# Kernel tuning notes

Measured on AMD Instinct MI355X. Metric: run time of the kernel, lower is better.

The kernel has to match this reference:

```python
import jax, jax.numpy as jnp
import numpy as np

GROUPS = 8   # channels // group_size with group_size=8 for C=64
EPS = 1e-5


def group_norm_qc(x0, x1, gamma, beta):
    """LatticeGroupNorm: stats computed jointly over both cosets per (batch, group)."""
    B, C, H, W = x0.shape
    g = GROUPS
    xg = jnp.concatenate([x0.reshape(B, g, -1), x1.reshape(B, g, -1)], axis=-1)
    mean = xg.mean(axis=-1).reshape(B, g, 1, 1, 1)
    var = xg.var(axis=-1).reshape(B, g, 1, 1, 1)
    inv = jax.lax.rsqrt(var + EPS)
    ga = gamma[None, :, None, None]
    be = beta[None, :, None, None]

    def norm(x):
        xr = x.reshape(B, g, C // g, H, W)
        return ((xr - mean) * inv).reshape(B, C, H, W) * ga + be

    return norm(x0), norm(x1)


def qc_conv(x0, x1, w_center, w_corner, bias):
    """Quincunx LatticePad+LatticeConvolution with stencil
    [(0,0),(2,0),(0,2),(2,2),(1,1)], center (1,1).
    w_center: [O,I] tap (1,1) (same-coset 1x1).
    w_corner: [O,I,2,2] taps (0,0),(2,0),(0,2),(2,2) (cross-coset 2x2).
    Pad keeps output cosets the same size as inputs ('same' lattice conv)."""
    dn = ('NCHW', 'OIHW', 'NCHW')

    def c1(x):
        return jnp.einsum('oi,bihw->bohw', w_center, x)

    def c2(x, pad):
        return jax.lax.conv_general_dilated(x, w_corner, (1, 1), pad,
                                            dimension_numbers=dn)

    b = bias[None, :, None, None]
    # coset0 output gathers coset1 at (i-1+a, j-1+b) -> pad top/left
    out0 = c1(x0) + c2(x1, ((1, 0), (1, 0))) + b
    # coset1 output gathers coset0 at (i+a, j+b) -> pad bottom/right
    out1 = c1(x1) + c2(x0, ((0, 1), (0, 1))) + b
    return out0, out1


def setup_inputs() -> dict:
    key = jax.random.key(0)
    ks = jax.random.split(key, 10)
    B, C, H, W = 2, 64, 256, 256
    s = 0.05
    return {
        'x0': jax.random.normal(ks[0], (B, C, H, W), jnp.float32),
        'x1': jax.random.normal(ks[1], (B, C, H, W), jnp.float32),
        'g1': jnp.ones((C,), jnp.float32),
        'b1': jnp.zeros((C,), jnp.float32),
        'w1_center': jax.random.normal(ks[2], (C, C), jnp.float32) * s,
        'w1_corner': jax.random.normal(ks[3], (C, C, 2, 2), jnp.float32) * s,
        'bias1': jax.random.normal(ks[4], (C,), jnp.float32) * s,
        'g2': jnp.ones((C,), jnp.float32),
        'b2': jnp.zeros((C,), jnp.float32),
        'w2_center': jax.random.normal(ks[5], (C, C), jnp.float32) * s,
        'w2_corner': jax.random.normal(ks[6], (C, C, 2, 2), jnp.float32) * s,
        'bias2': jax.random.normal(ks[7], (C,), jnp.float32) * s,
        'w_skip': jax.random.normal(ks[8], (C, C), jnp.float32) * s,
        'bias_skip': jax.random.normal(ks[9], (C,), jnp.float32) * s,
        'g_skip': jnp.ones((C,), jnp.float32),
        'beta_skip': jnp.zeros((C,), jnp.float32),
    }


def reference(x0, x1, g1, b1, w1_center, w1_corner, bias1,
              g2, b2, w2_center, w2_corner, bias2,
              w_skip, bias_skip, g_skip, beta_skip):
    # conv path: GN -> ReLU -> pad+conv -> GN -> ReLU -> pad+conv
    h0, h1 = group_norm_qc(x0, x1, g1, b1)
    h0, h1 = jax.nn.relu(h0), jax.nn.relu(h1)
    h0, h1 = qc_conv(h0, h1, w1_center, w1_corner, bias1)
    h0, h1 = group_norm_qc(h0, h1, g2, b2)
    h0, h1 = jax.nn.relu(h0), jax.nn.relu(h1)
    h0, h1 = qc_conv(h0, h1, w2_center, w2_corner, bias2)
    # skip path: 1x1 lattice conv (stencil [(0,0)]) -> GN
    bsk = bias_skip[None, :, None, None]
    s0 = jnp.einsum('oi,bihw->bohw', w_skip, x0) + bsk
    s1 = jnp.einsum('oi,bihw->bohw', w_skip, x1) + bsk
    s0, s1 = group_norm_qc(s0, s1, g_skip, beta_skip)
    # residual add; stack the two cosets as leading axis for a single output
    return jnp.stack([h0 + s0, h1 + s1])
```

## Files before the change

### kernel.cpp

```cpp
#include <hip/hip_runtime.h>

typedef __attribute__((ext_vector_type(8))) __bf16 bf16x8;
typedef __attribute__((ext_vector_type(4))) __bf16 bf16x4;
typedef __attribute__((ext_vector_type(4))) float f32x4;

#define MFMA16(a,b,c) __builtin_amdgcn_mfma_f32_16x16x32_bf16(a,b,c,0,0,0)

static constexpr int HW = 65536;
static constexpr int WD = 256;
static constexpr int NB = 2;
static constexpr double INV_N = 1.0 / 1048576.0;
static constexpr float EPSV = 1e-5f;

static constexpr size_t OFF_P1  = 0;
static constexpr size_t OFF_P2  = 131072;
static constexpr size_t OFF_A1  = 200704;
static constexpr size_t OFF_A2  = OFF_A1 + 40960;
static constexpr size_t OFF_XT  = OFF_A2 + 40960;
static constexpr size_t SZ_T    = (size_t)2 * NB * HW * 64 * 2;
static constexpr size_t OFF_S   = OFF_XT + SZ_T;
static constexpr size_t OFF_H   = OFF_S + SZ_T;

#define TL8(base, px, c) (*(const bf16x8*)&(base)[(px) * 64 + (((c)) ^ ((((px)) & 7) << 3))])

__global__ __launch_bounds__(256, 4) void K1(
    const float* __restrict__ x0, const float* __restrict__ x1,
    const float* __restrict__ wskip, const float* __restrict__ bskip,
    const float* __restrict__ wc1, const float* __restrict__ wk1,
    const float* __restrict__ wc2, const float* __restrict__ wk2,
    __bf16* __restrict__ xt, __bf16* __restrict__ sout,
    __bf16* __restrict__ A1, __bf16* __restrict__ A2, float* __restrict__ p1) {
  const int bx = blockIdx.x;
  const int t = threadIdx.x;

  if (bx >= 1024) {
    const int stage = bx - 1024;
    const float* wc = stage ? wc2 : wc1;
    const float* wk = stage ? wk2 : wk1;
    __bf16* A = stage ? A2 : A1;
    for (int idx = t; idx < 64 * 320; idx += 256) {
      int o = idx / 320, k = idx - o * 320;
      float v;
      if (k < 64) v = wc[o * 64 + k];
      else {
        int tp = (k - 64) >> 6;
        int c = k & 63;
        v = wk[(o * 64 + c) * 4 + tp];
      }
      A[idx] = (__bf16)v;
    }
    return;
  }

  const int row = bx & 255;
  const int b   = (bx >> 8) & 1;
  const int co  = bx >> 9;
  const float* x = co ? x1 : x0;
  __shared__ __attribute__((aligned(16))) __bf16 tile[256 * 64];
  __shared__ float redp[256];
  __shared__ float reds[32];
  const int wv = t >> 6, lane = t & 63;

  const float* xbase = x + (size_t)b * 64 * HW + (size_t)row * WD + t;
  __bf16* xtbase = xt + (((size_t)(co * NB + b) * HW) + (size_t)row * WD + t) * 64;

  float gsum[8], gsq[8];
#pragma unroll
  for (int g = 0; g < 8; ++g) { gsum[g] = 0.f; gsq[g] = 0.f; }
#pragma unroll
  for (int hf = 0; hf < 2; ++hf) {
    float f[32];
#pragma unroll
    for (int k = 0; k < 32; ++k) f[k] = xbase[(size_t)(hf * 32 + k) * HW];
    __builtin_amdgcn_sched_barrier(0);
#pragma unroll
    for (int c4 = 0; c4 < 4; ++c4) {
      const int cg = hf * 4 + c4;
      bf16x8 v;
#pragma unroll
      for (int j = 0; j < 8; ++j) {
        float xv = f[c4 * 8 + j];
        v[j] = (__bf16)xv;
        gsum[cg] += xv;
        gsq[cg] = fmaf(xv, xv, gsq[cg]);
      }
      *(bf16x8*)&tile[t * 64 + ((cg ^ (t & 7)) * 8)] = v;
      *(bf16x8*)&xtbase[cg * 8] = v;
    }
  }
#pragma unroll
  for (int g = 0; g < 8; ++g) {
#pragma unroll
    for (int m = 1; m < 16; m <<= 1) {
      gsum[g] += __shfl_xor(gsum[g], m, 64);
      gsq[g]  += __shfl_xor(gsq[g], m, 64);
    }
  }
  {
    const int q0 = lane >> 4;
    if ((lane & 15) == 0) {
#pragma unroll
      for (int g = 0; g < 8; ++g) {
        redp[(wv * 4 + q0) * 16 + g] = gsum[g];
        redp[(wv * 4 + q0) * 16 + 8 + g] = gsq[g];
      }
    }
  }
  __syncthreads();

  const int ln = lane & 15, q = lane >> 4;
  const int ch0 = wv * 16 + q * 4;
  bf16x8 a0, a1;
#pragma unroll
  for (int j = 0; j < 8; ++j) {
    a0[j] = (__bf16)wskip[(wv * 16 + ln) * 64 + q * 8 + j];
    a1[j] = (__bf16)wskip[(wv * 16 + ln) * 64 + 32 + q * 8 + j];
  }
  float bia[4];
#pragma unroll
  for (int r = 0; r < 4; ++r) bia[r] = bskip[ch0 + r];

  float ssum = 0.f, ssq = 0.f;
  for (int n = 0; n < 16; ++n) {
    f32x4 acc = {0.f, 0.f, 0.f, 0.f};
    const int px = n * 16 + ln;
    bf16x8 b0 = TL8(tile, px, q * 8);
    bf16x8 b1 = TL8(tile, px, q * 8 + 32);
    acc = MFMA16(a0, b0, acc);
    acc = MFMA16(a1, b1, acc);
    bf16x4 sv;
    float v[4];
#pragma unroll
    for (int r = 0; r < 4; ++r) {
      v[r] = acc[r] + bia[r];
      ssum += v[r];
      ssq = fmaf(v[r], v[r], ssq);
      sv[r] = (__bf16)v[r];
    }
    size_t sb = ((size_t)(co * NB + b) * 4096 + row * 16 + n) * 1024 + (wv * 4 + q) * 64 + ln * 4;
    *(bf16x4*)&sout[sb] = sv;
  }
#pragma unroll
  for (int m = 1; m < 16; m <<= 1) {
    ssum += __shfl_xor(ssum, m, 64);
    ssq  += __shfl_xor(ssq, m, 64);
  }
  if ((lane & 15) == 0) {
    reds[wv * 4 + q] = ssum;
    reds[16 + wv * 4 + q] = ssq;
  }

  __syncthreads();
  if (t < 32) {
    float val;
    if (t < 16) {
      val = 0.f;
#pragma unroll
      for (int k = 0; k < 16; ++k) val += redp[k * 16 + t];
    } else {
      int kind = (t >> 3) & 1, g = t & 7;
      int wvv = g >> 1, qp = g & 1;
      val = reds[kind * 16 + wvv * 4 + qp * 2] + reds[kind * 16 + wvv * 4 + qp * 2 + 1];
    }
    const int bf1 = (co * 2 + b) * 256 + row;
    p1[(size_t)bf1 * 32 + t] = val;
  }
}

__global__ __launch_bounds__(256, 4) void K2(
    const __bf16* __restrict__ xt, const __bf16* __restrict__ A1,
    const float* __restrict__ p1, const float* __restrict__ g1, const float* __restrict__ be1,
    const float* __restrict__ bias1,
    __bf16* __restrict__ h, float* __restrict__ p2) {
  const int blk = ((blockIdx.x & 7) << 6) | (blockIdx.x >> 3);
  const int tx = blk & 15, ty = blk >> 4;
  const int b = blockIdx.y;
  const int y0p = ty * 8, x0p = tx * 16;
  __shared__ __attribute__((aligned(16))) __bf16 tl[2][153 * 64];
  __shared__ float sc[64], sh[64];
  __shared__ float lst[16];
  __shared__ double redn[16];
  const int t = threadIdx.x;

  bf16x8 raw[10];
#pragma unroll
  for (int i = 0; i < 10; ++i) {
    int u = t + i * 256;
    int cs = (u >= 1224) ? 1 : 0;
    int rr = u - cs * 1224;
    int px = rr >> 3, cg = rr & 7;
    int ly = px / 17, lx = px - ly * 17;
    int gy = y0p + ly - cs, gx = x0p + lx - cs;
    if (u < 2448 && (unsigned)gy < 256u && (unsigned)gx < 256u)
      raw[i] = *(const bf16x8*)&xt[(((size_t)(cs * NB + b) * WD + gy) * WD + gx) * 64 + cg * 8];
  }
  __builtin_amdgcn_sched_barrier(0);

  if (t < 16) lst[t] = 0.f;
  {
    const int col = t >> 4, sub = t & 15;
    double v = 0.0;
    for (int j = sub; j < 512; j += 16) {
      int cc = j >> 8, rr2 = j & 255;
      v += (double)p1[((size_t)(cc * 2 + b) * 256 + rr2) * 32 + col];
    }
    v += __shfl_xor(v, 1, 64);
    v += __shfl_xor(v, 2, 64);
    v += __shfl_xor(v, 4, 64);
    v += __shfl_xor(v, 8, 64);
    if (sub == 0) redn[col] = v;
  }
  __syncthreads();
  if (t < 64) {
    int g = t >> 3;
    double mean = redn[g] * INV_N;
    double var  = redn[8 + g] * INV_N - mean * mean;
    float inv = rsqrtf((float)var + EPSV);
    float s_ = inv * g1[t];
    sc[t] = s_;
    sh[t] = be1[t] - (float)mean * s_;
  }
  __syncthreads();

#pragma unroll
  for (int i = 0; i < 10; ++i) {
    int u = t + i * 256;
    int cs = (u >= 1224) ? 1 : 0;
    int rr = u - cs * 1224;
    int px = rr >> 3, cg = rr & 7;
    int ly = px / 17, lx = px - ly * 17;
    int gy = y0p + ly - cs, gx = x0p + lx - cs;
    if (u < 2448) {
      bool inb = (unsigned)gy < 256u && (unsigned)gx < 256u;
      bf16x8 v;
#pragma unroll
      for (int j = 0; j < 8; ++j) {
        float fv = inb ? fmaf((float)raw[i][j], sc[cg * 8 + j], sh[cg * 8 + j]) : 0.f;
        v[j] = (__bf16)fmaxf(fv, 0.f);
      }
      *(bf16x8*)&tl[cs][px * 64 + ((cg ^ (px & 7)) * 8)] = v;
    }
  }

  const int wv = t >> 6, lane = t & 63, ln = lane & 15, q = lane >> 4;
  const int co = wv & 1, mh = wv >> 1;
  const int q8 = q * 8;
  bf16x8 af[2][10];
#pragma unroll
  for (int m = 0; m < 2; ++m)
#pragma unroll
    for (int kk = 0; kk < 10; ++kk)
      af[m][kk] = *(const bf16x8*)&A1[(mh * 32 + m * 16 + ln) * 320 + kk * 32 + q8];
  __syncthreads();

  f32x4 acc[8][2];
#pragma unroll
  for (int n = 0; n < 8; ++n)
#pragma unroll
    for (int m = 0; m < 2; ++m) acc[n][m] = (f32x4){0.f, 0.f, 0.f, 0.f};

  const __bf16* tc = tl[co];
  const __bf16* to = tl[1 - co];
#pragma unroll
  for (int n = 0; n < 8; ++n) {
    const int cpix = co ? ((n + 1) * 17 + ln + 1) : (n * 17 + ln);
    const int tb = n * 17 + ln;
    bf16x8 bb;
    bb = TL8(tc, cpix, q8);          acc[n][0]=MFMA16(af[0][0],bb,acc[n][0]); acc[n][1]=MFMA16(af[1][0],bb,acc[n][1]);
    bb = TL8(tc, cpix, q8 + 32);     acc[n][0]=MFMA16(af[0][1],bb,acc[n][0]); acc[n][1]=MFMA16(af[1][1],bb,acc[n][1]);
    bb = TL8(to, tb, q8);            acc[n][0]=MFMA16(af[0][2],bb,acc[n][0]); acc[n][1]=MFMA16(af[1][2],bb,acc[n][1]);
    bb = TL8(to, tb, q8 + 32);       acc[n][0]=MFMA16(af[0][3],bb,acc[n][0]); acc[n][1]=MFMA16(af[1][3],bb,acc[n][1]);
    bb = TL8(to, tb + 1, q8);        acc[n][0]=MFMA16(af[0][4],bb,acc[n][0]); acc[n][1]=MFMA16(af[1][4],bb,acc[n][1]);
    bb = TL8(to, tb + 1, q8 + 32);   acc[n][0]=MFMA16(af[0][5],bb,acc[n][0]); acc[n][1]=MFMA16(af[1][5],bb,acc[n][1]);
    bb = TL8(to, tb + 17, q8);       acc[n][0]=MFMA16(af[0][6],bb,acc[n][0]); acc[n][1]=MFMA16(af[1][6],bb,acc[n][1]);
    bb = TL8(to, tb + 17, q8 + 32);  acc[n][0]=MFMA16(af[0][7],bb,acc[n][0]); acc[n][1]=MFMA16(af[1][7],bb,acc[n][1]);
    bb = TL8(to, tb + 18, q8);       acc[n][0]=MFMA16(af[0][8],bb,acc[n][0]); acc[n][1]=MFMA16(af[1][8],bb,acc[n][1]);
    bb = TL8(to, tb + 18, q8 + 32);  acc[n][0]=MFMA16(af[0][9],bb,acc[n][0]); acc[n][1]=MFMA16(af[1][9],bb,acc[n][1]);
  }

  __syncthreads();

  float s2s[2] = {0.f, 0.f}, s2q[2] = {0.f, 0.f};
  float bia[2][4];
#pragma unroll
  for (int m = 0; m < 2; ++m)
#pragma unroll
    for (int r = 0; r < 4; ++r) bia[m][r] = bias1[mh * 32 + m * 16 + q * 4 + r];

#pragma unroll
  for (int n = 0; n < 8; ++n)
#pragma unroll
    for (int m = 0; m < 2; ++m) {
      bf16x4 hv;
#pragma unroll
      for (int r = 0; r < 4; ++r) {
        float v = acc[n][m][r] + bia[m][r];
        s2s[m] += v;
        s2q[m] = fmaf(v, v, s2q[m]);
        hv[r] = (__bf16)v;
      }
      *(bf16x4*)&tl[co][(n * 16 + ln) * 64 + ((mh * 32 + m * 16 + q * 4) ^ ((ln & 7) << 3))] = hv;
    }

#pragma unroll
  for (int m = 0; m < 2; ++m) {
    float a_ = s2s[m], c_ = s2q[m];
#pragma unroll
    for (int mk = 1; mk < 32; mk <<= 1) {
      a_ += __shfl_xor(a_, mk, 64);
      c_ += __shfl_xor(c_, mk, 64);
    }
    if ((lane & 31) == 0) {
      int g = mh * 4 + m * 2 + (q >> 1);
      atomicAdd(&lst[g], a_);
      atomicAdd(&lst[8 + g], c_);
    }
  }
  __syncthreads();

#pragma unroll
  for (int i = 0; i < 8; ++i) {
    int co2 = i >> 2;
    int idx = (i & 3) * 256 + t;
    int px = idx >> 3, chunk = idx & 7;
    int gy = y0p + (px >> 4), gx = x0p + (px & 15);
    bf16x8 vv = *(const bf16x8*)&tl[co2][px * 64 + ((chunk ^ (px & 7)) * 8)];
    *(bf16x8*)&h[(((size_t)(co2 * NB + b) * WD + gy) * WD + gx) * 64 + chunk * 8] = vv;
  }

  if (t < 16) p2[((size_t)b * 512 + blockIdx.x) * 16 + t] = lst[t];
}

__global__ __launch_bounds__(256, 4) void K3(
    const __bf16* __restrict__ hin, const __bf16* __restrict__ A2,
    const float* __restrict__ p2, const float* __restrict__ p1,
    const float* __restrict__ g2, const float* __restrict__ be2, const float* __restrict__ bias2,
    const float* __restrict__ gsk, const float* __restrict__ besk,
    const __bf16* __restrict__ sin_, float* __restrict__ out) {
  const int blk = ((blockIdx.x & 7) << 6) | (blockIdx.x >> 3);
  const int tx = blk & 15, ty = blk >> 4;
  const int b = blockIdx.y;
  const int y0p = ty * 8, x0p = tx * 16;
  __shared__ __attribute__((aligned(16))) __bf16 tl[2][153 * 64];
  __shared__ float sc2[64], sh2[64], scS[64], shS[64];
  __shared__ double redn[32];
  const int t = threadIdx.x;

  bf16x8 raw[10];
#pragma unroll
  for (int i = 0; i < 10; ++i) {
    int u = t + i * 256;
    int cs = (u >= 1224) ? 1 : 0;
    int rr = u - cs * 1224;
    int px = rr >> 3, cg = rr & 7;
    int ly = px / 17, lx = px - ly * 17;
    int gy = y0p + ly - cs, gx = x0p + lx - cs;
    if (u < 2448 && (unsigned)gy < 256u && (unsigned)gx < 256u)
      raw[i] = *(const bf16x8*)&hin[(((size_t)(cs * NB + b) * WD + gy) * WD + gx) * 64 + cg * 8];
  }
  __builtin_amdgcn_sched_barrier(0);

  {
    const int col = t >> 3, sub = t & 7;
    double v = 0.0;
    if (col < 16) {
      for (int j = sub; j < 512; j += 8)
        v += (double)p2[((size_t)b * 512 + j) * 16 + col];
    } else {
      for (int j = sub; j < 512; j += 8) {
        int cc = j >> 8, rr2 = j & 255;
        v += (double)p1[((size_t)(cc * 2 + b) * 256 + rr2) * 32 + col];
      }
    }
    v += __shfl_xor(v, 1, 64);
    v += __shfl_xor(v, 2, 64);
    v += __shfl_xor(v, 4, 64);
    if (sub == 0) redn[col] = v;
  }
  __syncthreads();
  if (t < 128) {
    int half = t >> 6, ch = t & 63, g = ch >> 3;
    if (half == 0) {
      double mean = redn[g] * INV_N;
      double var  = redn[8 + g] * INV_N - mean * mean;
      float inv = rsqrtf((float)var + EPSV);
      float s_ = inv * g2[ch];
      sc2[ch] = s_;
      sh2[ch] = be2[ch] - (float)mean * s_;
    } else {
      double mean = redn[16 + g] * INV_N;
      double var  = redn[24 + g] * INV_N - mean * mean;
      float inv = rsqrtf((float)var + EPSV);
      float s_ = inv * gsk[ch];
      scS[ch] = s_;
      shS[ch] = besk[ch] - (float)mean * s_;
    }
  }
  __syncthreads();

#pragma unroll
  for (int i = 0; i < 10; ++i) {
    int u = t + i * 256;
    int cs = (u >= 1224) ? 1 : 0;
    int rr = u - cs * 1224;
    int px = rr >> 3, cg = rr & 7;
    int ly = px / 17, lx = px - ly * 17;
    int gy = y0p + ly - cs, gx = x0p + lx - cs;
    if (u < 2448) {
      bool inb = (unsigned)gy < 256u && (unsigned)gx < 256u;
      bf16x8 v;
#pragma unroll
      for (int j = 0; j < 8; ++j) {
        float fv = inb ? fmaf((float)raw[i][j], sc2[cg * 8 + j], sh2[cg * 8 + j]) : 0.f;
        v[j] = (__bf16)fmaxf(fv, 0.f);
      }
      *(bf16x8*)&tl[cs][px * 64 + ((cg ^ (px & 7)) * 8)] = v;
    }
  }

  const int wv = t >> 6, lane = t & 63, ln = lane & 15, q = lane >> 4;
  const int co = wv & 1, mh = wv >> 1;
  const int q8 = q * 8;
  bf16x8 af[2][10];
#pragma unroll
  for (int m = 0; m < 2; ++m)
#pragma unroll
    for (int kk = 0; kk < 10; ++kk)
      af[m][kk] = *(const bf16x8*)&A2[(mh * 32 + m * 16 + ln) * 320 + kk * 32 + q8];
  __syncthreads();

  f32x4 acc[8][2];
#pragma unroll
  for (int n = 0; n < 8; ++n)
#pragma unroll
    for (int m = 0; m < 2; ++m) acc[n][m] = (f32x4){0.f, 0.f, 0.f, 0.f};

  const __bf16* tc = tl[co];
  const __bf16* to = tl[1 - co];
#pragma unroll
  for (int n = 0; n < 8; ++n) {
    const int cpix = co ? ((n + 1) * 17 + ln + 1) : (n * 17 + ln);
    const int tb = n * 17 + ln;
    bf16x8 bb;
    bb = TL8(tc, cpix, q8);          acc[n][0]=MFMA16(af[0][0],bb,acc[n][0]); acc[n][1]=MFMA16(af[1][0],bb,acc[n][1]);
    bb = TL8(tc, cpix, q8 + 32);     acc[n][0]=MFMA16(af[0][1],bb,acc[n][0]); acc[n][1]=MFMA16(af[1][1],bb,acc[n][1]);
    bb = TL8(to, tb, q8);            acc[n][0]=MFMA16(af[0][2],bb,acc[n][0]); acc[n][1]=MFMA16(af[1][2],bb,acc[n][1]);
    bb = TL8(to, tb, q8 + 32);       acc[n][0]=MFMA16(af[0][3],bb,acc[n][0]); acc[n][1]=MFMA16(af[1][3],bb,acc[n][1]);
    bb = TL8(to, tb + 1, q8);        acc[n][0]=MFMA16(af[0][4],bb,acc[n][0]); acc[n][1]=MFMA16(af[1][4],bb,acc[n][1]);
    bb = TL8(to, tb + 1, q8 + 32);   acc[n][0]=MFMA16(af[0][5],bb,acc[n][0]); acc[n][1]=MFMA16(af[1][5],bb,acc[n][1]);
    bb = TL8(to, tb + 17, q8);       acc[n][0]=MFMA16(af[0][6],bb,acc[n][0]); acc[n][1]=MFMA16(af[1][6],bb,acc[n][1]);
    bb = TL8(to, tb + 17, q8 + 32);  acc[n][0]=MFMA16(af[0][7],bb,acc[n][0]); acc[n][1]=MFMA16(af[1][7],bb,acc[n][1]);
    bb = TL8(to, tb + 18, q8);       acc[n][0]=MFMA16(af[0][8],bb,acc[n][0]); acc[n][1]=MFMA16(af[1][8],bb,acc[n][1]);
    bb = TL8(to, tb + 18, q8 + 32);  acc[n][0]=MFMA16(af[0][9],bb,acc[n][0]); acc[n][1]=MFMA16(af[1][9],bb,acc[n][1]);
  }

  float bia[2][4], sA[2][4], sB[2][4];
#pragma unroll
  for (int m = 0; m < 2; ++m)
#pragma unroll
    for (int r = 0; r < 4; ++r) {
      int ch = mh * 32 + m * 16 + q * 4 + r;
      bia[m][r] = bias2[ch];
      sA[m][r] = scS[ch];
      sB[m][r] = shS[ch];
    }

#pragma unroll
  for (int ng = 0; ng < 2; ++ng) {
    bf16x4 sv[4][2];
#pragma unroll
    for (int nn = 0; nn < 4; ++nn) {
      int n = ng * 4 + nn;
      int gy = y0p + n;
#pragma unroll
      for (int m = 0; m < 2; ++m)
        sv[nn][m] = *(const bf16x4*)&sin_[((size_t)(co * NB + b) * 4096 + gy * 16 + tx) * 1024 + (mh * 8 + m * 4 + q) * 64 + ln * 4];
    }
    __builtin_amdgcn_sched_barrier(0);
#pragma unroll
    for (int nn = 0; nn < 4; ++nn) {
      int n = ng * 4 + nn;
      int gy = y0p + n;
#pragma unroll
      for (int m = 0; m < 2; ++m) {
        int ch0 = mh * 32 + m * 16 + q * 4;
        size_t ob = ((size_t)(co * NB + b) * 64 + ch0) * HW + (size_t)gy * WD + x0p + ln;
#pragma unroll
        for (int r = 0; r < 4; ++r) {
          float v = acc[n][m][r] + bia[m][r] + fmaf((float)sv[nn][m][r], sA[m][r], sB[m][r]);
          out[ob + (size_t)r * HW] = v;
        }
      }
    }
  }
}

extern "C" void kernel_launch(void* const* d_in, const int* in_sizes, int n_in,
                              void* d_out, int out_size, void* d_ws, size_t ws_size,
                              hipStream_t stream) {
  (void)in_sizes; (void)n_in; (void)out_size; (void)ws_size;
  const float* x0    = (const float*)d_in[0];
  const float* x1    = (const float*)d_in[1];
  const float* g1    = (const float*)d_in[2];
  const float* b1    = (const float*)d_in[3];
  const float* w1c   = (const float*)d_in[4];
  const float* w1k   = (const float*)d_in[5];
  const float* bias1 = (const float*)d_in[6];
  const float* g2    = (const float*)d_in[7];
  const float* b2    = (const float*)d_in[8];
  const float* w2c   = (const float*)d_in[9];
  const float* w2k   = (const float*)d_in[10];
  const float* bias2 = (const float*)d_in[11];
  const float* wsk   = (const float*)d_in[12];
  const float* bsk   = (const float*)d_in[13];
  const float* gsk   = (const float*)d_in[14];
  const float* besk  = (const float*)d_in[15];

  char* ws = (char*)d_ws;
  float*  p1 = (float*)(ws + OFF_P1);
  float*  p2 = (float*)(ws + OFF_P2);
  __bf16* A1 = (__bf16*)(ws + OFF_A1);
  __bf16* A2 = (__bf16*)(ws + OFF_A2);
  __bf16* xt = (__bf16*)(ws + OFF_XT);
  __bf16* s  = (__bf16*)(ws + OFF_S);
  __bf16* h  = (__bf16*)(ws + OFF_H);

  K1<<<dim3(1026), 256, 0, stream>>>(x0, x1, wsk, bsk, w1c, w1k, w2c, w2k, xt, s, A1, A2, p1);
  K2<<<dim3(512, 2), 256, 0, stream>>>(xt, A1, p1, g1, b1, bias1, h, p2);
  K3<<<dim3(512, 2), 256, 0, stream>>>(h, A2, p2, p1, g2, b2, bias2, gsk, besk, s, (float*)d_out);
}
```

Baseline: 309.1 us.

## Fuse three kernels into one cooperative persistent kernel with grid syncs

Adds a cooperative kernel KF that runs the stats/skip-conv stage, the first GN+conv stage and the second GN+conv+residual stage in a single launch. The stages are separated by grid.sync() and share one reused shared-memory buffer. Weight repacking is spread across all blocks instead of two extra blocks. The goal is to remove launch gaps and kernel-boundary drains between the three stages, at the cost of grid-barrier overhead. It also requires all 1024 blocks to be co-resident (4 per CU), and falls back to the old three-kernel path otherwise.

```diff
diff --git a/kernel.cpp b/kernel.cpp
--- a/kernel.cpp
+++ b/kernel.cpp
@@ -1,4 +1,7 @@
 #include <hip/hip_runtime.h>
+#include <hip/hip_cooperative_groups.h>
+
+namespace cg = cooperative_groups;
 
 typedef __attribute__((ext_vector_type(8))) __bf16 bf16x8;
 typedef __attribute__((ext_vector_type(4))) __bf16 bf16x4;
@@ -22,6 +25,459 @@
 static constexpr size_t OFF_H   = OFF_S + SZ_T;
 
 #define TL8(base, px, c) (*(const bf16x8*)&(base)[(px) * 64 + (((c)) ^ ((((px)) & 7) << 3))])
+
+__global__ __launch_bounds__(256, 4) void KF(
+    const float* __restrict__ x0, const float* __restrict__ x1,
+    const float* __restrict__ wskip, const float* __restrict__ bskip,
+    const float* __restrict__ wc1, const float* __restrict__ wk1,
+    const float* __restrict__ wc2, const float* __restrict__ wk2,
+    const float* __restrict__ g1, const float* __restrict__ be1, const float* __restrict__ bias1,
+    const float* __restrict__ g2, const float* __restrict__ be2, const float* __restrict__ bias2,
+    const float* __restrict__ gsk, const float* __restrict__ besk,
+    __bf16* __restrict__ xt, __bf16* __restrict__ sout, __bf16* __restrict__ h,
+    __bf16* __restrict__ A1, __bf16* __restrict__ A2,
+    float* __restrict__ p1, float* __restrict__ p2, float* __restrict__ out) {
+  cg::grid_group grid = cg::this_grid();
+  __shared__ __attribute__((aligned(16))) char smem[40448];
+  const int bx = blockIdx.x;
+  const int t = threadIdx.x;
+  const int wv = t >> 6, lane = t & 63;
+  const int ln = lane & 15, q = lane >> 4;
+  const int q8 = q * 8;
+
+  {
+    __bf16* tile = (__bf16*)smem;
+    float* redp  = (float*)(smem + 32768);
+    float* reds  = (float*)(smem + 33792);
+
+    if (t < 40) {
+      int e = bx * 40 + t;
+      int stage = e / 20480, idx = e - stage * 20480;
+      const float* wc = stage ? wc2 : wc1;
+      const float* wk = stage ? wk2 : wk1;
+      int o = idx / 320, k = idx - o * 320;
+      float v = (k < 64) ? wc[o * 64 + k] : wk[(o * 64 + (k & 63)) * 4 + ((k - 64) >> 6)];
+      (stage ? A2 : A1)[idx] = (__bf16)v;
+    }
+
+    const int row = bx & 255, b = (bx >> 8) & 1, co = bx >> 9;
+    const float* x = co ? x1 : x0;
+    const float* xbase = x + (size_t)b * 64 * HW + (size_t)row * WD + t;
+    __bf16* xtbase = xt + (((size_t)(co * NB + b) * HW) + (size_t)row * WD + t) * 64;
+
+    float gsum[8], gsq[8];
+#pragma unroll
+    for (int g = 0; g < 8; ++g) { gsum[g] = 0.f; gsq[g] = 0.f; }
+#pragma unroll
+    for (int hf = 0; hf < 2; ++hf) {
+      float f[32];
+#pragma unroll
+      for (int k = 0; k < 32; ++k) f[k] = xbase[(size_t)(hf * 32 + k) * HW];
+      __builtin_amdgcn_sched_barrier(0);
+#pragma unroll
+      for (int c4 = 0; c4 < 4; ++c4) {
+        const int cgi = hf * 4 + c4;
+        bf16x8 v;
+#pragma unroll
+        for (int j = 0; j < 8; ++j) {
+          float xv = f[c4 * 8 + j];
+          v[j] = (__bf16)xv;
+          gsum[cgi] += xv;
+          gsq[cgi] = fmaf(xv, xv, gsq[cgi]);
+        }
+        *(bf16x8*)&tile[t * 64 + ((cgi ^ (t & 7)) * 8)] = v;
+        *(bf16x8*)&xtbase[cgi * 8] = v;
+      }
+    }
+#pragma unroll
+    for (int g = 0; g < 8; ++g) {
+#pragma unroll
+      for (int m = 1; m < 16; m <<= 1) {
+        gsum[g] += __shfl_xor(gsum[g], m, 64);
+        gsq[g]  += __shfl_xor(gsq[g], m, 64);
+      }
+    }
+    if ((lane & 15) == 0) {
+#pragma unroll
+      for (int g = 0; g < 8; ++g) {
+        redp[(wv * 4 + q) * 16 + g] = gsum[g];
+        redp[(wv * 4 + q) * 16 + 8 + g] = gsq[g];
+      }
+    }
+    __syncthreads();
+
+    bf16x8 a0, a1;
+#pragma unroll
+    for (int j = 0; j < 8; ++j) {
+      a0[j] = (__bf16)wskip[(wv * 16 + ln) * 64 + q * 8 + j];
+      a1[j] = (__bf16)wskip[(wv * 16 + ln) * 64 + 32 + q * 8 + j];
+    }
+    float bia[4];
+#pragma unroll
+    for (int r = 0; r < 4; ++r) bia[r] = bskip[wv * 16 + q * 4 + r];
+
+    float ssum = 0.f, ssq = 0.f;
+    for (int n = 0; n < 16; ++n) {
+      f32x4 acc = {0.f, 0.f, 0.f, 0.f};
+      const int px = n * 16 + ln;
+      bf16x8 b0 = TL8(tile, px, q * 8);
+      bf16x8 b1 = TL8(tile, px, q * 8 + 32);
+      acc = MFMA16(a0, b0, acc);
+      acc = MFMA16(a1, b1, acc);
+      bf16x4 sv;
+#pragma unroll
+      for (int r = 0; r < 4; ++r) {
+        float v = acc[r] + bia[r];
+        ssum += v;
+        ssq = fmaf(v, v, ssq);
+        sv[r] = (__bf16)v;
+      }
+      size_t sb = ((size_t)(co * NB + b) * 4096 + row * 16 + n) * 1024 + (wv * 4 + q) * 64 + ln * 4;
+      *(bf16x4*)&sout[sb] = sv;
+    }
+#pragma unroll
+    for (int m = 1; m < 16; m <<= 1) {
+      ssum += __shfl_xor(ssum, m, 64);
+      ssq  += __shfl_xor(ssq, m, 64);
+    }
+    if ((lane & 15) == 0) {
+      reds[wv * 4 + q] = ssum;
+      reds[16 + wv * 4 + q] = ssq;
+    }
+    __syncthreads();
+    if (t < 32) {
+      float val;
+      if (t < 16) {
+        val = 0.f;
+#pragma unroll
+        for (int k = 0; k < 16; ++k) val += redp[k * 16 + t];
+      } else {
+        int kind = (t >> 3) & 1, g = t & 7;
+        int wvv = g >> 1, qp = g & 1;
+        val = reds[kind * 16 + wvv * 4 + qp * 2] + reds[kind * 16 + wvv * 4 + qp * 2 + 1];
+      }
+      p1[(size_t)((co * 2 + b) * 256 + row) * 32 + t] = val;
+    }
+  }
+
+  grid.sync();
+
+  const int gidx = ((bx & 7) << 7) | (bx >> 3);
+  const int b23 = gidx >> 9, r23 = gidx & 511;
+  const int tx = r23 & 15, ty = r23 >> 4;
+  const int y0p = ty * 8, x0p = tx * 16;
+  __bf16* tl0 = (__bf16*)smem;
+  __bf16* tl1 = tl0 + 153 * 64;
+
+  {
+    float* sc   = (float*)(smem + 39168);
+    float* sh   = (float*)(smem + 39424);
+    float* lst  = (float*)(smem + 39680);
+    double* redn = (double*)(smem + 39744);
+
+    bf16x8 raw[10];
+#pragma unroll
+    for (int i = 0; i < 10; ++i) {
+      int u = t + i * 256;
+      int cs = (u >= 1224) ? 1 : 0;
+      int rr = u - cs * 1224;
+      int px = rr >> 3, cgi = rr & 7;
+      int ly = px / 17, lx = px - ly * 17;
+      int gy = y0p + ly - cs, gx = x0p + lx - cs;
+      if (u < 2448 && (unsigned)gy < 256u && (unsigned)gx < 256u)
+        raw[i] = *(const bf16x8*)&xt[(((size_t)(cs * NB + b23) * WD + gy) * WD + gx) * 64 + cgi * 8];
+    }
+    __builtin_amdgcn_sched_barrier(0);
+
+    if (t < 16) lst[t] = 0.f;
+    {
+      const int col = t >> 4, sub = t & 15;
+      double v = 0.0;
+      for (int j = sub; j < 512; j += 16) {
+        int cc = j >> 8, rr2 = j & 255;
+        v += (double)p1[((size_t)(cc * 2 + b23) * 256 + rr2) * 32 + col];
+      }
+      v += __shfl_xor(v, 1, 64);
+      v += __shfl_xor(v, 2, 64);
+      v += __shfl_xor(v, 4, 64);
+      v += __shfl_xor(v, 8, 64);
+      if (sub == 0) redn[col] = v;
+    }
+    __syncthreads();
+    if (t < 64) {
+      int g = t >> 3;
+      double mean = redn[g] * INV_N;
+      double var  = redn[8 + g] * INV_N - mean * mean;
+      float inv = rsqrtf((float)var + EPSV);
+      float s_ = inv * g1[t];
+      sc[t] = s_;
+      sh[t] = be1[t] - (float)mean * s_;
+    }
+    __syncthreads();
+
+#pragma unroll
+    for (int i = 0; i < 10; ++i) {
+      int u = t + i * 256;
+      int cs = (u >= 1224) ? 1 : 0;
+      int rr = u - cs * 1224;
+      int px = rr >> 3, cgi = rr & 7;
+      int ly = px / 17, lx = px - ly * 17;
+      int gy = y0p + ly - cs, gx = x0p + lx - cs;
+      if (u < 2448) {
+        bool inb = (unsigned)gy < 256u && (unsigned)gx < 256u;
+        bf16x8 v;
+#pragma unroll
+        for (int j = 0; j < 8; ++j) {
+          float fv = inb ? fmaf((float)raw[i][j], sc[cgi * 8 + j], sh[cgi * 8 + j]) : 0.f;
+          v[j] = (__bf16)fmaxf(fv, 0.f);
+        }
+        *(bf16x8*)&(cs ? tl1 : tl0)[px * 64 + ((cgi ^ (px & 7)) * 8)] = v;
+      }
+    }
+
+    const int co = wv & 1, mh = wv >> 1;
+    bf16x8 af[2][10];
+#pragma unroll
+    for (int m = 0; m < 2; ++m)
+#pragma unroll
+      for (int kk = 0; kk < 10; ++kk)
+        af[m][kk] = *(const bf16x8*)&A1[(mh * 32 + m * 16 + ln) * 320 + kk * 32 + q8];
+    __syncthreads();
+
+    f32x4 acc[8][2];
+#pragma unroll
+    for (int n = 0; n < 8; ++n)
+#pragma unroll
+      for (int m = 0; m < 2; ++m) acc[n][m] = (f32x4){0.f, 0.f, 0.f, 0.f};
+
+    const __bf16* tc = co ? tl1 : tl0;
+    const __bf16* to = co ? tl0 : tl1;
+#pragma unroll
+    for (int n = 0; n < 8; ++n) {
+      const int cpix = co ? ((n + 1) * 17 + ln + 1) : (n * 17 + ln);
+      const int tb = n * 17 + ln;
+      bf16x8 bb;
+      bb = TL8(tc, cpix, q8);          acc[n][0]=MFMA16(af[0][0],bb,acc[n][0]); acc[n][1]=MFMA16(af[1][0],bb,acc[n][1]);
+      bb = TL8(tc, cpix, q8 + 32);     acc[n][0]=MFMA16(af[0][1],bb,acc[n][0]); acc[n][1]=MFMA16(af[1][1],bb,acc[n][1]);
+      bb = TL8(to, tb, q8);            acc[n][0]=MFMA16(af[0][2],bb,acc[n][0]); acc[n][1]=MFMA16(af[1][2],bb,acc[n][1]);
+      bb = TL8(to, tb, q8 + 32);       acc[n][0]=MFMA16(af[0][3],bb,acc[n][0]); acc[n][1]=MFMA16(af[1][3],bb,acc[n][1]);
+      bb = TL8(to, tb + 1, q8);        acc[n][0]=MFMA16(af[0][4],bb,acc[n][0]); acc[n][1]=MFMA16(af[1][4],bb,acc[n][1]);
+      bb = TL8(to, tb + 1, q8 + 32);   acc[n][0]=MFMA16(af[0][5],bb,acc[n][0]); acc[n][1]=MFMA16(af[1][5],bb,acc[n][1]);
+      bb = TL8(to, tb + 17, q8);       acc[n][0]=MFMA16(af[0][6],bb,acc[n][0]); acc[n][1]=MFMA16(af[1][6],bb,acc[n][1]);
+      bb = TL8(to, tb + 17, q8 + 32);  acc[n][0]=MFMA16(af[0][7],bb,acc[n][0]); acc[n][1]=MFMA16(af[1][7],bb,acc[n][1]);
+      bb = TL8(to, tb + 18, q8);       acc[n][0]=MFMA16(af[0][8],bb,acc[n][0]); acc[n][1]=MFMA16(af[1][8],bb,acc[n][1]);
+      bb = TL8(to, tb + 18, q8 + 32);  acc[n][0]=MFMA16(af[0][9],bb,acc[n][0]); acc[n][1]=MFMA16(af[1][9],bb,acc[n][1]);
+    }
+
+    __syncthreads();
+
+    float s2s[2] = {0.f, 0.f}, s2q[2] = {0.f, 0.f};
+    float bia[2][4];
+#pragma unroll
+    for (int m = 0; m < 2; ++m)
+#pragma unroll
+      for (int r = 0; r < 4; ++r) bia[m][r] = bias1[mh * 32 + m * 16 + q * 4 + r];
+
+#pragma unroll
+    for (int n = 0; n < 8; ++n)
+#pragma unroll
+      for (int m = 0; m < 2; ++m) {
+        bf16x4 hv;
+#pragma unroll
+        for (int r = 0; r < 4; ++r) {
+          float v = acc[n][m][r] + bia[m][r];
+          s2s[m] += v;
+          s2q[m] = fmaf(v, v, s2q[m]);
+          hv[r] = (__bf16)v;
+        }
+        *(bf16x4*)&(co ? tl1 : tl0)[(n * 16 + ln) * 64 + ((mh * 32 + m * 16 + q * 4) ^ ((ln & 7) << 3))] = hv;
+      }
+
+#pragma unroll
+    for (int m = 0; m < 2; ++m) {
+      float a_ = s2s[m], c_ = s2q[m];
+#pragma unroll
+      for (int mk = 1; mk < 32; mk <<= 1) {
+        a_ += __shfl_xor(a_, mk, 64);
+        c_ += __shfl_xor(c_, mk, 64);
+      }
+      if ((lane & 31) == 0) {
+        int g = mh * 4 + m * 2 + (q >> 1);
+        atomicAdd(&lst[g], a_);
+        atomicAdd(&lst[8 + g], c_);
+      }
+    }
+    __syncthreads();
+
+#pragma unroll
+    for (int i = 0; i < 8; ++i) {
+      int co2 = i >> 2;
+      int idx = (i & 3) * 256 + t;
+      int px = idx >> 3, chunk = idx & 7;
+      int gy = y0p + (px >> 4), gx = x0p + (px & 15);
+      bf16x8 vv = *(const bf16x8*)&(co2 ? tl1 : tl0)[px * 64 + ((chunk ^ (px & 7)) * 8)];
+      *(bf16x8*)&h[(((size_t)(co2 * NB + b23) * WD + gy) * WD + gx) * 64 + chunk * 8] = vv;
+    }
+
+    if (t < 16) p2[((size_t)b23 * 512 + r23) * 16 + t] = lst[t];
+  }
+
+  grid.sync();
+
+  {
+    float* sc2  = (float*)(smem + 39168);
+    float* sh2  = (float*)(smem + 39424);
+    float* scS  = (float*)(smem + 39680);
+    float* shS  = (float*)(smem + 39936);
+    double* redn = (double*)(smem + 40192);
+
+    bf16x8 raw[10];
+#pragma unroll
+    for (int i = 0; i < 10; ++i) {
+      int u = t + i * 256;
+      int cs = (u >= 1224) ? 1 : 0;
+      int rr = u - cs * 1224;
+      int px = rr >> 3, cgi = rr & 7;
+      int ly = px / 17, lx = px - ly * 17;
+      int gy = y0p + ly - cs, gx = x0p + lx - cs;
+      if (u < 2448 && (unsigned)gy < 256u && (unsigned)gx < 256u)
+        raw[i] = *(const bf16x8*)&h[(((size_t)(cs * NB + b23) * WD + gy) * WD + gx) * 64 + cgi * 8];
+    }
+    __builtin_amdgcn_sched_barrier(0);
+
+    {
+      const int col = t >> 3, sub = t & 7;
+      double v = 0.0;
+      if (col < 16) {
+        for (int j = sub; j < 512; j += 8)
+          v += (double)p2[((size_t)b23 * 512 + j) * 16 + col];
+      } else {
+        for (int j = sub; j < 512; j += 8) {
+          int cc = j >> 8, rr2 = j & 255;
+          v += (double)p1[((size_t)(cc * 2 + b23) * 256 + rr2) * 32 + col];
+        }
+      }
+      v += __shfl_xor(v, 1, 64);
+      v += __shfl_xor(v, 2, 64);
+      v += __shfl_xor(v, 4, 64);
+      if (sub == 0) redn[col] = v;
+    }
+    __syncthreads();
+    if (t < 128) {
+      int half = t >> 6, ch = t & 63, g = ch >> 3;
+      if (half == 0) {
+        double mean = redn[g] * INV_N;
+        double var  = redn[8 + g] * INV_N - mean * mean;
+        float inv = rsqrtf((float)var + EPSV);
+        float s_ = inv * g2[ch];
+        sc2[ch] = s_;
+        sh2[ch] = be2[ch] - (float)mean * s_;
+      } else {
+        double mean = redn[16 + g] * INV_N;
+        double var  = redn[24 + g] * INV_N - mean * mean;
+        float inv = rsqrtf((float)var + EPSV);
+        float s_ = inv * gsk[ch];
+        scS[ch] = s_;
+        shS[ch] = besk[ch] - (float)mean * s_;
+      }
+    }
+    __syncthreads();
+
+#pragma unroll
+    for (int i = 0; i < 10; ++i) {
+      int u = t + i * 256;
+      int cs = (u >= 1224) ? 1 : 0;
+      int rr = u - cs * 1224;
+      int px = rr >> 3, cgi = rr & 7;
+      int ly = px / 17, lx = px - ly * 17;
+      int gy = y0p + ly - cs, gx = x0p + lx - cs;
+      if (u < 2448) {
+        bool inb = (unsigned)gy < 256u && (unsigned)gx < 256u;
+        bf16x8 v;
+#pragma unroll
+        for (int j = 0; j < 8; ++j) {
+          float fv = inb ? fmaf((float)raw[i][j], sc2[cgi * 8 + j], sh2[cgi * 8 + j]) : 0.f;
+          v[j] = (__bf16)fmaxf(fv, 0.f);
+        }
+        *(bf16x8*)&(cs ? tl1 : tl0)[px * 64 + ((cgi ^ (px & 7)) * 8)] = v;
+      }
+    }
+
+    const int co = wv & 1, mh = wv >> 1;
+    bf16x8 af[2][10];
+#pragma unroll
+    for (int m = 0; m < 2; ++m)
+#pragma unroll
+      for (int kk = 0; kk < 10; ++kk)
+        af[m][kk] = *(const bf16x8*)&A2[(mh * 32 + m * 16 + ln) * 320 + kk * 32 + q8];
+    __syncthreads();
+
+    f32x4 acc[8][2];
+#pragma unroll
+    for (int n = 0; n < 8; ++n)
+#pragma unroll
+      for (int m = 0; m < 2; ++m) acc[n][m] = (f32x4){0.f, 0.f, 0.f, 0.f};
+
+    const __bf16* tc = co ? tl1 : tl0;
+    const __bf16* to = co ? tl0 : tl1;
+#pragma unroll
+    for (int n = 0; n < 8; ++n) {
+      const int cpix = co ? ((n + 1) * 17 + ln + 1) : (n * 17 + ln);
+      const int tb = n * 17 + ln;
+      bf16x8 bb;
+      bb = TL8(tc, cpix, q8);          acc[n][0]=MFMA16(af[0][0],bb,acc[n][0]); acc[n][1]=MFMA16(af[1][0],bb,acc[n][1]);
+      bb = TL8(tc, cpix, q8 + 32);     acc[n][0]=MFMA16(af[0][1],bb,acc[n][0]); acc[n][1]=MFMA16(af[1][1],bb,acc[n][1]);
+      bb = TL8(to, tb, q8);            acc[n][0]=MFMA16(af[0][2],bb,acc[n][0]); acc[n][1]=MFMA16(af[1][2],bb,acc[n][1]);
+      bb = TL8(to, tb, q8 + 32);       acc[n][0]=MFMA16(af[0][3],bb,acc[n][0]); acc[n][1]=MFMA16(af[1][3],bb,acc[n][1]);
+      bb = TL8(to, tb + 1, q8);        acc[n][0]=MFMA16(af[0][4],bb,acc[n][0]); acc[n][1]=MFMA16(af[1][4],bb,acc[n][1]);
+      bb = TL8(to, tb + 1, q8 + 32);   acc[n][0]=MFMA16(af[0][5],bb,acc[n][0]); acc[n][1]=MFMA16(af[1][5],bb,acc[n][1]);
+      bb = TL8(to, tb + 17, q8);       acc[n][0]=MFMA16(af[0][6],bb,acc[n][0]); acc[n][1]=MFMA16(af[1][6],bb,acc[n][1]);
+      bb = TL8(to, tb + 17, q8 + 32);  acc[n][0]=MFMA16(af[0][7],bb,acc[n][0]); acc[n][1]=MFMA16(af[1][7],bb,acc[n][1]);
+      bb = TL8(to, tb + 18, q8);       acc[n][0]=MFMA16(af[0][8],bb,acc[n][0]); acc[n][1]=MFMA16(af[1][8],bb,acc[n][1]);
+      bb = TL8(to, tb + 18, q8 + 32);  acc[n][0]=MFMA16(af[0][9],bb,acc[n][0]); acc[n][1]=MFMA16(af[1][9],bb,acc[n][1]);
+    }
+
+    float bia[2][4], sA[2][4], sB[2][4];
+#pragma unroll
+    for (int m = 0; m < 2; ++m)
+#pragma unroll
+      for (int r = 0; r < 4; ++r) {
+        int ch = mh * 32 + m * 16 + q * 4 + r;
+        bia[m][r] = bias2[ch];
+        sA[m][r] = scS[ch];
+        sB[m][r] = shS[ch];
+      }
+
+#pragma unroll
+    for (int ng = 0; ng < 2; ++ng) {
+      bf16x4 sv[4][2];
+#pragma unroll
+      for (int nn = 0; nn < 4; ++nn) {
+        int n = ng * 4 + nn;
+        int gy = y0p + n;
+#pragma unroll
+        for (int m = 0; m < 2; ++m)
+          sv[nn][m] = *(const bf16x4*)&sout[((size_t)(co * NB + b23) * 4096 + gy * 16 + tx) * 1024 + (mh * 8 + m * 4 + q) * 64 + ln * 4];
+      }
+      __builtin_amdgcn_sched_barrier(0);
+#pragma unroll
+      for (int nn = 0; nn < 4; ++nn) {
+        int n = ng * 4 + nn;
+        int gy = y0p + n;
+#pragma unroll
+        for (int m = 0; m < 2; ++m) {
+          int ch0 = mh * 32 + m * 16 + q * 4;
+          size_t ob = ((size_t)(co * NB + b23) * 64 + ch0) * HW + (size_t)gy * WD + x0p + ln;
+#pragma unroll
+          for (int r = 0; r < 4; ++r) {
+            float v = acc[n][m][r] + bia[m][r] + fmaf((float)sv[nn][m][r], sA[m][r], sB[m][r]);
+            out[ob + (size_t)r * HW] = v;
+          }
+        }
+      }
+    }
+  }
+}
 
 __global__ __launch_bounds__(256, 4) void K1(
     const float* __restrict__ x0, const float* __restrict__ x1,
@@ -32,7 +488,6 @@
     __bf16* __restrict__ A1, __bf16* __restrict__ A2, float* __restrict__ p1) {
   const int bx = blockIdx.x;
   const int t = threadIdx.x;
-
   if (bx >= 1024) {
     const int stage = bx - 1024;
     const float* wc = stage ? wc2 : wc1;
@@ -42,28 +497,19 @@
       int o = idx / 320, k = idx - o * 320;
       float v;
       if (k < 64) v = wc[o * 64 + k];
-      else {
-        int tp = (k - 64) >> 6;
-        int c = k & 63;
-        v = wk[(o * 64 + c) * 4 + tp];
-      }
+      else v = wk[(o * 64 + (k & 63)) * 4 + ((k - 64) >> 6)];
       A[idx] = (__bf16)v;
     }
     return;
   }
-
-  const int row = bx & 255;
-  const int b   = (bx >> 8) & 1;
-  const int co  = bx >> 9;
+  const int row = bx & 255, b = (bx >> 8) & 1, co = bx >> 9;
   const float* x = co ? x1 : x0;
   __shared__ __attribute__((aligned(16))) __bf16 tile[256 * 64];
   __shared__ float redp[256];
   __shared__ float reds[32];
   const int wv = t >> 6, lane = t & 63;
-
   const float* xbase = x + (size_t)b * 64 * HW + (size_t)row * WD + t;
   __bf16* xtbase = xt + (((size_t)(co * NB + b) * HW) + (size_t)row * WD + t) * 64;
-
   float gsum[8], gsq[8];
 #pragma unroll
   for (int g = 0; g < 8; ++g) { gsum[g] = 0.f; gsq[g] = 0.f; }
@@ -107,9 +553,7 @@
     }
   }
   __syncthreads();
-
   const int ln = lane & 15, q = lane >> 4;
-  const int ch0 = wv * 16 + q * 4;
   bf16x8 a0, a1;
 #pragma unroll
   for (int j = 0; j < 8; ++j) {
@@ -118,8 +562,7 @@
   }
   float bia[4];
 #pragma unroll
-  for (int r = 0; r < 4; ++r) bia[r] = bskip[ch0 + r];
-
+  for (int r = 0; r < 4; ++r) bia[r] = bskip[wv * 16 + q * 4 + r];
   float ssum = 0.f, ssq = 0.f;
   for (int n = 0; n < 16; ++n) {
     f32x4 acc = {0.f, 0.f, 0.f, 0.f};
@@ -129,13 +572,12 @@
     acc = MFMA16(a0, b0, acc);
     acc = MFMA16(a1, b1, acc);
     bf16x4 sv;
-    float v[4];
 #pragma unroll
     for (int r = 0; r < 4; ++r) {
-      v[r] = acc[r] + bia[r];
-      ssum += v[r];
-      ssq = fmaf(v[r], v[r], ssq);
-      sv[r] = (__bf16)v[r];
+      float v = acc[r] + bia[r];
+      ssum += v;
+      ssq = fmaf(v, v, ssq);
+      sv[r] = (__bf16)v;
     }
     size_t sb = ((size_t)(co * NB + b) * 4096 + row * 16 + n) * 1024 + (wv * 4 + q) * 64 + ln * 4;
     *(bf16x4*)&sout[sb] = sv;
@@ -149,7 +591,6 @@
     reds[wv * 4 + q] = ssum;
     reds[16 + wv * 4 + q] = ssq;
   }
-
   __syncthreads();
   if (t < 32) {
     float val;
@@ -162,8 +603,7 @@
       int wvv = g >> 1, qp = g & 1;
       val = reds[kind * 16 + wvv * 4 + qp * 2] + reds[kind * 16 + wvv * 4 + qp * 2 + 1];
     }
-    const int bf1 = (co * 2 + b) * 256 + row;
-    p1[(size_t)bf1 * 32 + t] = val;
+    p1[(size_t)((co * 2 + b) * 256 + row) * 32 + t] = val;
   }
 }
 
@@ -181,7 +621,6 @@
   __shared__ float lst[16];
   __shared__ double redn[16];
   const int t = threadIdx.x;
-
   bf16x8 raw[10];
 #pragma unroll
   for (int i = 0; i < 10; ++i) {
@@ -195,7 +634,6 @@
       raw[i] = *(const bf16x8*)&xt[(((size_t)(cs * NB + b) * WD + gy) * WD + gx) * 64 + cg * 8];
   }
   __builtin_amdgcn_sched_barrier(0);
-
   if (t < 16) lst[t] = 0.f;
   {
     const int col = t >> 4, sub = t & 15;
@@ -221,7 +659,6 @@
     sh[t] = be1[t] - (float)mean * s_;
   }
   __syncthreads();
-
 #pragma unroll
   for (int i = 0; i < 10; ++i) {
     int u = t + i * 256;
@@ -241,7 +678,6 @@
       *(bf16x8*)&tl[cs][px * 64 + ((cg ^ (px & 7)) * 8)] = v;
     }
   }
-
   const int wv = t >> 6, lane = t & 63, ln = lane & 15, q = lane >> 4;
   const int co = wv & 1, mh = wv >> 1;
   const int q8 = q * 8;
@@ -252,13 +688,11 @@
     for (int kk = 0; kk < 10; ++kk)
       af[m][kk] = *(const bf16x8*)&A1[(mh * 32 + m * 16 + ln) * 320 + kk * 32 + q8];
   __syncthreads();
-
   f32x4 acc[8][2];
 #pragma unroll
   for (int n = 0; n < 8; ++n)
 #pragma unroll
     for (int m = 0; m < 2; ++m) acc[n][m] = (f32x4){0.f, 0.f, 0.f, 0.f};
-
   const __bf16* tc = tl[co];
   const __bf16* to = tl[1 - co];
 #pragma unroll
@@ -277,16 +711,13 @@
     bb = TL8(to, tb + 18, q8);       acc[n][0]=MFMA16(af[0][8],bb,acc[n][0]); acc[n][1]=MFMA16(af[1][8],bb,acc[n][1]);
     bb = TL8(to, tb + 18, q8 + 32);  acc[n][0]=MFMA16(af[0][9],bb,acc[n][0]); acc[n][1]=MFMA16(af[1][9],bb,acc[n][1]);
   }
-
   __syncthreads();
-
   float s2s[2] = {0.f, 0.f}, s2q[2] = {0.f, 0.f};
   float bia[2][4];
 #pragma unroll
   for (int m = 0; m < 2; ++m)
 #pragma unroll
     for (int r = 0; r < 4; ++r) bia[m][r] = bias1[mh * 32 + m * 16 + q * 4 + r];
-
 #pragma unroll
   for (int n = 0; n < 8; ++n)
 #pragma unroll
@@ -301,7 +732,6 @@
       }
       *(bf16x4*)&tl[co][(n * 16 + ln) * 64 + ((mh * 32 + m * 16 + q * 4) ^ ((ln & 7) << 3))] = hv;
     }
-
 #pragma unroll
   for (int m = 0; m < 2; ++m) {
     float a_ = s2s[m], c_ = s2q[m];
@@ -317,7 +747,6 @@
     }
   }
   __syncthreads();
-
 #pragma unroll
   for (int i = 0; i < 8; ++i) {
     int co2 = i >> 2;
@@ -327,7 +756,6 @@
     bf16x8 vv = *(const bf16x8*)&tl[co2][px * 64 + ((chunk ^ (px & 7)) * 8)];
     *(bf16x8*)&h[(((size_t)(co2 * NB + b) * WD + gy) * WD + gx) * 64 + chunk * 8] = vv;
   }
-
   if (t < 16) p2[((size_t)b * 512 + blockIdx.x) * 16 + t] = lst[t];
 }
 
@@ -345,7 +773,6 @@
   __shared__ float sc2[64], sh2[64], scS[64], shS[64];
   __shared__ double redn[32];
   const int t = threadIdx.x;
-
   bf16x8 raw[10];
 #pragma unroll
   for (int i = 0; i < 10; ++i) {
@@ -359,7 +786,6 @@
       raw[i] = *(const bf16x8*)&hin[(((size_t)(cs * NB + b) * WD + gy) * WD + gx) * 64 + cg * 8];
   }
   __builtin_amdgcn_sched_barrier(0);
-
   {
     const int col = t >> 3, sub = t & 7;
     double v = 0.0;
@@ -397,7 +823,6 @@
     }
   }
   __syncthreads();
-
 #pragma unroll
   for (int i = 0; i < 10; ++i) {
     int u = t + i * 256;
@@ -417,7 +842,6 @@
       *(bf16x8*)&tl[cs][px * 64 + ((cg ^ (px & 7)) * 8)] = v;
     }
   }
-
   const int wv = t >> 6, lane = t & 63, ln = lane & 15, q = lane >> 4;
   const int co = wv & 1, mh = wv >> 1;
   const int q8 = q * 8;
@@ -428,13 +852,11 @@
     for (int kk = 0; kk < 10; ++kk)
       af[m][kk] = *(const bf16x8*)&A2[(mh * 32 + m * 16 + ln) * 320 + kk * 32 + q8];
   __syncthreads();
-
   f32x4 acc[8][2];
 #pragma unroll
   for (int n = 0; n < 8; ++n)
 #pragma unroll
     for (int m = 0; m < 2; ++m) acc[n][m] = (f32x4){0.f, 0.f, 0.f, 0.f};
-
   const __bf16* tc = tl[co];
   const __bf16* to = tl[1 - co];
 #pragma unroll
@@ -453,7 +875,6 @@
     bb = TL8(to, tb + 18, q8);       acc[n][0]=MFMA16(af[0][8],bb,acc[n][0]); acc[n][1]=MFMA16(af[1][8],bb,acc[n][1]);
     bb = TL8(to, tb + 18, q8 + 32);  acc[n][0]=MFMA16(af[0][9],bb,acc[n][0]); acc[n][1]=MFMA16(af[1][9],bb,acc[n][1]);
   }
-
   float bia[2][4], sA[2][4], sB[2][4];
 #pragma unroll
   for (int m = 0; m < 2; ++m)
@@ -464,7 +885,6 @@
       sA[m][r] = scS[ch];
       sB[m][r] = shS[ch];
     }
-
 #pragma unroll
   for (int ng = 0; ng < 2; ++ng) {
     bf16x4 sv[4][2];
@@ -524,8 +944,32 @@
   __bf16* xt = (__bf16*)(ws + OFF_XT);
   __bf16* s  = (__bf16*)(ws + OFF_S);
   __bf16* h  = (__bf16*)(ws + OFF_H);
+  float* outp = (float*)d_out;
+
+  static int coopOK = -1;
+  if (coopOK < 0) {
+    int nb = 0;
+    hipError_t e = hipOccupancyMaxActiveBlocksPerMultiprocessor(&nb, KF, 256, 0);
+    coopOK = (e == hipSuccess && nb >= 4) ? 1 : 0;
+  }
+
+  if (coopOK) {
+    void* kargs[] = {
+      (void*)&x0, (void*)&x1, (void*)&wsk, (void*)&bsk,
+      (void*)&w1c, (void*)&w1k, (void*)&w2c, (void*)&w2k,
+      (void*)&g1, (void*)&b1, (void*)&bias1,
+      (void*)&g2, (void*)&b2, (void*)&bias2,
+      (void*)&gsk, (void*)&besk,
+      (void*)&xt, (void*)&s, (void*)&h, (void*)&A1, (void*)&A2,
+      (void*)&p1, (void*)&p2, (void*)&outp
+    };
+    hipError_t e = hipLaunchCooperativeKernel((void*)KF, dim3(1024), dim3(256),
+                                              kargs, 0, stream);
+    if (e == hipSuccess) return;
+    coopOK = 0;
+  }
 
   K1<<<dim3(1026), 256, 0, stream>>>(x0, x1, wsk, bsk, w1c, w1k, w2c, w2k, xt, s, A1, A2, p1);
   K2<<<dim3(512, 2), 256, 0, stream>>>(xt, A1, p1, g1, b1, bias1, h, p2);
-  K3<<<dim3(512, 2), 256, 0, stream>>>(h, A2, p2, p1, g2, b2, bias2, gsk, besk, s, (float*)d_out);
+  K3<<<dim3(512, 2), 256, 0, stream>>>(h, A2, p2, p1, g2, b2, bias2, gsk, besk, s, outp);
 }
```

Result: no change. 309.2 us (+0.0%).
